# Performance work log

Measured on AMD Instinct MI355X. Metric: run time of the kernel, lower is better.

Reference implementation:

```python
import jax, jax.numpy as jnp
import numpy as np
from itertools import combinations

ADD = 3  # matches init_kwargs

def setup_inputs() -> dict:
    key = jax.random.key(0)
    x = jax.random.uniform(key, (131072, 16), dtype=jnp.float32)
    return {"x": x}

def reference(x) -> jnp.ndarray:
    n = x.shape[1]
    parts = [x]
    for i in range(2, ADD + 1):
        # static index table of all size-i column subsets: [C(n,i), i]
        idx = jnp.asarray(np.array(list(combinations(range(n), i)), dtype=np.int32))
        # gather + reduce: x[:, idx] -> [N, C, i]; Lukasiewicz t-norm = max(sum - (i-1), 0)
        s = jnp.sum(x[:, idx], axis=2)  # [N, C]
        parts.append(jnp.maximum(s - jnp.float32(i - 1), jnp.float32(0)))
    return jnp.concatenate(parts, axis=1)
```

## Files before the change

### kernel.cpp

```cpp
#include <hip/hip_runtime.h>


#define NCOLS 696
#define NC4   174
#define RPT   16
#define QPT   (RPT * NC4)

typedef float v4f __attribute__((ext_vector_type(4)));

struct ColTab { unsigned int v[NCOLS]; };

constexpr ColTab make_tab() {
    ColTab t{};
    int k = 0;
    for (int a = 0; a < 16; ++a)
        t.v[k++] = (unsigned)a | (16u << 5) | (16u << 10);
    for (int a = 0; a < 16; ++a)
        for (int b = a + 1; b < 16; ++b)
            t.v[k++] = (unsigned)a | ((unsigned)b << 5) | (16u << 10) | (1u << 15);
    for (int a = 0; a < 16; ++a)
        for (int b = a + 1; b < 16; ++b)
            for (int c = b + 1; c < 16; ++c)
                t.v[k++] = (unsigned)a | ((unsigned)b << 5) | ((unsigned)c << 10) | (2u << 15);
    return t;
}

__constant__ ColTab g_tab = make_tab();

__device__ __forceinline__ float tnorm(const float* __restrict__ xr, unsigned v) {
    return fmaxf(xr[v & 31u] + xr[(v >> 5) & 31u] + xr[(v >> 10) & 31u]
                 - (float)((v >> 15) & 3u), 0.0f);
}

__global__ __launch_bounds__(256) void luk_kernel(const float* __restrict__ x,
                                                  float* __restrict__ out,
                                                  int nrows, int ntiles) {
    __shared__ float xl[RPT * 17];
    const int t = threadIdx.x;
    const uint4* __restrict__ tab4 = reinterpret_cast<const uint4*>(g_tab.v);
    v4f* __restrict__ out4 = reinterpret_cast<v4f*>(out);

    for (int tile = blockIdx.x; tile < ntiles; tile += gridDim.x) {
        const int row0 = tile * RPT;
        const int rlim = min(RPT, nrows - row0);

        {
            const int r = t >> 4, a = t & 15;
            float v = 0.0f;
            if (r < rlim) v = x[(size_t)row0 * 16 + t];
            xl[r * 17 + a] = v;
            if (t < RPT) xl[t * 17 + 16] = 0.0f;
        }
        __syncthreads();

        const int nq = rlim * NC4;
        const size_t qbase = (size_t)row0 * NC4;
        for (int i = t; i < nq; i += 256) {
            const int r  = (unsigned)i / (unsigned)NC4;
            const int c4 = i - r * NC4;
            const uint4 tv = tab4[c4];
            const float* __restrict__ xr = &xl[r * 17];
            v4f o;
            o.x = tnorm(xr, tv.x);
            o.y = tnorm(xr, tv.y);
            o.z = tnorm(xr, tv.z);
            o.w = tnorm(xr, tv.w);
            out4[qbase + i] = o;
        }
        __syncthreads();
    }
}

extern "C" void kernel_launch(void* const* d_in, const int* in_sizes, int n_in,
                              void* d_out, int out_size, void* d_ws, size_t ws_size,
                              hipStream_t stream) {
    const float* x = (const float*)d_in[0];
    float* out = (float*)d_out;
    const int nrows  = in_sizes[0] / 16;
    const int ntiles = (nrows + RPT - 1) / RPT;
    const int blocks = ntiles < 2048 ? ntiles : 2048;
    luk_kernel<<<blocks, 256, 0, stream>>>(x, out, nrows, ntiles);
}
```

Measured before the change: 372.9 us.

## Compute one row per thread in registers with compile-time column table and LDS transpose

Each thread now loads its whole 16-float row into registers. All 696 outputs are generated through template-unrolled compile-time index tables, which removes the per-element table lookups, indirect LDS reads and integer division. Results are staged per wave in LDS in groups of 32 columns and transposed, so stores go out as contiguous 128-byte segments. The grid is now one thread per row, with no bounds check, so it assumes the row count is a multiple of 256. Code size and register use rise.

New measurement: 447.9 us. 20.1% more time.

```diff
diff --git a/kernel.cpp b/kernel.cpp
--- a/kernel.cpp
+++ b/kernel.cpp
@@ -3,72 +3,88 @@
 
 #define NCOLS 696
 #define NC4   174
-#define RPT   16
-#define QPT   (RPT * NC4)
+#define NG    22
 
 typedef float v4f __attribute__((ext_vector_type(4)));
 
-struct ColTab { unsigned int v[NCOLS]; };
-
-constexpr ColTab make_tab() {
-    ColTab t{};
+struct Tabs { signed char a[NCOLS], b[NCOLS], c[NCOLS], t[NCOLS]; };
+constexpr Tabs make_tabs() {
+    Tabs T{};
     int k = 0;
+    for (int a = 0; a < 16; ++a) {
+        T.a[k] = (signed char)a; T.b[k] = 0; T.c[k] = 0; T.t[k] = 0; ++k;
+    }
     for (int a = 0; a < 16; ++a)
-        t.v[k++] = (unsigned)a | (16u << 5) | (16u << 10);
+        for (int b = a + 1; b < 16; ++b) {
+            T.a[k] = (signed char)a; T.b[k] = (signed char)b; T.c[k] = 0; T.t[k] = 1; ++k;
+        }
     for (int a = 0; a < 16; ++a)
         for (int b = a + 1; b < 16; ++b)
-            t.v[k++] = (unsigned)a | ((unsigned)b << 5) | (16u << 10) | (1u << 15);
-    for (int a = 0; a < 16; ++a)
-        for (int b = a + 1; b < 16; ++b)
-            for (int c = b + 1; c < 16; ++c)
-                t.v[k++] = (unsigned)a | ((unsigned)b << 5) | ((unsigned)c << 10) | (2u << 15);
-    return t;
+            for (int c = b + 1; c < 16; ++c) {
+                T.a[k] = (signed char)a; T.b[k] = (signed char)b;
+                T.c[k] = (signed char)c; T.t[k] = 2; ++k;
+            }
+    return T;
+}
+constexpr Tabs TT = make_tabs();
+
+template<int COL>
+__device__ __forceinline__ float elem(const float* __restrict__ xr) {
+    constexpr int A = TT.a[COL], B = TT.b[COL], C = TT.c[COL], TY = TT.t[COL];
+    if constexpr (TY == 0)      return xr[A];
+    else if constexpr (TY == 1) return fmaxf(xr[A] + xr[B] - 1.0f, 0.0f);
+    else                        return fmaxf((xr[A] + xr[B]) + xr[C] - 2.0f, 0.0f);
 }
 
-__constant__ ColTab g_tab = make_tab();
+template<int G, int J, int NQ>
+__device__ __forceinline__ void compute_quads(const float* __restrict__ xr,
+                                              v4f* __restrict__ slab, int lane) {
+    if constexpr (J < NQ) {
+        constexpr int col0 = 32 * G + 4 * J;
+        v4f o;
+        o.x = elem<col0 + 0>(xr);
+        o.y = elem<col0 + 1>(xr);
+        o.z = elem<col0 + 2>(xr);
+        o.w = elem<col0 + 3>(xr);
+        slab[J * 64 + lane] = o;
+        compute_quads<G, J + 1, NQ>(xr, slab, lane);
+    }
+}
 
-__device__ __forceinline__ float tnorm(const float* __restrict__ xr, unsigned v) {
-    return fmaxf(xr[v & 31u] + xr[(v >> 5) & 31u] + xr[(v >> 10) & 31u]
-                 - (float)((v >> 15) & 3u), 0.0f);
+template<int G>
+__device__ __forceinline__ void do_group(const float* __restrict__ xr,
+                                         v4f* __restrict__ slab, int lane,
+                                         v4f* __restrict__ blk4, int voffq) {
+    constexpr int NQ = (G < 21) ? 8 : 6;
+    compute_quads<G, 0, NQ>(xr, slab, lane);
+    #pragma unroll
+    for (int m = 0; m < 8; ++m) {
+        const v4f o = slab[(lane & 7) * 64 + m * 8 + (lane >> 3)];
+        if (NQ == 8 || (lane & 7) < NQ)
+            blk4[voffq + m * (8 * NC4) + G * 8] = o;
+    }
+    if constexpr (G + 1 < NG) do_group<G + 1>(xr, slab, lane, blk4, voffq);
 }
 
 __global__ __launch_bounds__(256) void luk_kernel(const float* __restrict__ x,
                                                   float* __restrict__ out,
-                                                  int nrows, int ntiles) {
-    __shared__ float xl[RPT * 17];
+                                                  int nrows) {
+    __shared__ v4f slab[4][8 * 64];
     const int t = threadIdx.x;
-    const uint4* __restrict__ tab4 = reinterpret_cast<const uint4*>(g_tab.v);
-    v4f* __restrict__ out4 = reinterpret_cast<v4f*>(out);
+    const int w = t >> 6, lane = t & 63;
+    const int row0 = blockIdx.x * 256 + w * 64;
+    const int row  = row0 + lane;
 
-    for (int tile = blockIdx.x; tile < ntiles; tile += gridDim.x) {
-        const int row0 = tile * RPT;
-        const int rlim = min(RPT, nrows - row0);
+    float xr[16];
+    const v4f* __restrict__ xv = reinterpret_cast<const v4f*>(x) + (size_t)row * 4;
+    *reinterpret_cast<v4f*>(&xr[0])  = xv[0];
+    *reinterpret_cast<v4f*>(&xr[4])  = xv[1];
+    *reinterpret_cast<v4f*>(&xr[8])  = xv[2];
+    *reinterpret_cast<v4f*>(&xr[12]) = xv[3];
 
-        {
-            const int r = t >> 4, a = t & 15;
-            float v = 0.0f;
-            if (r < rlim) v = x[(size_t)row0 * 16 + t];
-            xl[r * 17 + a] = v;
-            if (t < RPT) xl[t * 17 + 16] = 0.0f;
-        }
-        __syncthreads();
-
-        const int nq = rlim * NC4;
-        const size_t qbase = (size_t)row0 * NC4;
-        for (int i = t; i < nq; i += 256) {
-            const int r  = (unsigned)i / (unsigned)NC4;
-            const int c4 = i - r * NC4;
-            const uint4 tv = tab4[c4];
-            const float* __restrict__ xr = &xl[r * 17];
-            v4f o;
-            o.x = tnorm(xr, tv.x);
-            o.y = tnorm(xr, tv.y);
-            o.z = tnorm(xr, tv.z);
-            o.w = tnorm(xr, tv.w);
-            out4[qbase + i] = o;
-        }
-        __syncthreads();
-    }
+    v4f* __restrict__ blk4 = reinterpret_cast<v4f*>(out) + (size_t)row0 * NC4;
+    const int voffq = (lane >> 3) * NC4 + (lane & 7);
+    do_group<0>(xr, slab[w], lane, blk4, voffq);
 }
 
 extern "C" void kernel_launch(void* const* d_in, const int* in_sizes, int n_in,
@@ -77,7 +93,6 @@
     const float* x = (const float*)d_in[0];
     float* out = (float*)d_out;
     const int nrows  = in_sizes[0] / 16;
-    const int ntiles = (nrows + RPT - 1) / RPT;
-    const int blocks = ntiles < 2048 ? ntiles : 2048;
-    luk_kernel<<<blocks, 256, 0, stream>>>(x, out, nrows, ntiles);
+    const int blocks = nrows / 256;
+    luk_kernel<<<blocks, 256, 0, stream>>>(x, out, nrows);
 }
```

## Precompute pair sums in LDS and hoist per-thread column offsets into registers

Applied to the files above, without the earlier changes.

Each row's 120 pairwise sums are computed once into shared memory, and each triple is then evaluated as a pair sum plus a single column, so every output needs two LDS reads instead of three. Per-thread packed byte offsets and biases are computed once before the tile loop and held in registers, which removes the constant-table loads and the div/mod from the inner loop. The partial-tile handling is dropped, so correctness assumes the row count is a multiple of 16. This adds an extra barrier and phase per tile and raises register use.

New measurement: 368.2 us. About the same (-1.3%).

```diff
diff --git a/kernel.cpp b/kernel.cpp
--- a/kernel.cpp
+++ b/kernel.cpp
@@ -4,68 +4,119 @@
 #define NCOLS 696
 #define NC4   174
 #define RPT   16
-#define QPT   (RPT * NC4)
+#define RSTR  260
+#define ZOFF  256
+#define NQ    (RPT * NC4)
+#define KITER 11
 
 typedef float v4f __attribute__((ext_vector_type(4)));
 
-struct ColTab { unsigned int v[NCOLS]; };
-
-constexpr ColTab make_tab() {
-    ColTab t{};
+struct DTab { unsigned int v[NCOLS]; };
+constexpr DTab make_dtab() {
+    DTab d{};
+    int pidx[16][16] = {};
+    int pi = 0;
+    for (int a = 0; a < 16; ++a)
+        for (int b = a + 1; b < 16; ++b) pidx[a][b] = pi++;
     int k = 0;
     for (int a = 0; a < 16; ++a)
-        t.v[k++] = (unsigned)a | (16u << 5) | (16u << 10);
+        d.v[k++] = (unsigned)(a * 4) | ((unsigned)(ZOFF * 4) << 16);
     for (int a = 0; a < 16; ++a)
         for (int b = a + 1; b < 16; ++b)
-            t.v[k++] = (unsigned)a | ((unsigned)b << 5) | (16u << 10) | (1u << 15);
+            d.v[k++] = (unsigned)((136 + pidx[a][b]) * 4) | ((unsigned)(ZOFF * 4) << 16);
     for (int a = 0; a < 16; ++a)
         for (int b = a + 1; b < 16; ++b)
             for (int c = b + 1; c < 16; ++c)
-                t.v[k++] = (unsigned)a | ((unsigned)b << 5) | ((unsigned)c << 10) | (2u << 15);
-    return t;
+                d.v[k++] = (unsigned)((16 + pidx[a][b]) * 4) | ((unsigned)(c * 4) << 16);
+    return d;
 }
+__constant__ DTab g_dtab = make_dtab();
 
-__constant__ ColTab g_tab = make_tab();
+struct PTab { unsigned short v[120]; };
+constexpr PTab make_ptab() {
+    PTab p{};
+    int k = 0;
+    for (int a = 0; a < 16; ++a)
+        for (int b = a + 1; b < 16; ++b)
+            p.v[k++] = (unsigned short)((a * 4) | ((b * 4) << 8));
+    return p;
+}
+__constant__ PTab g_ptab = make_ptab();
 
-__device__ __forceinline__ float tnorm(const float* __restrict__ xr, unsigned v) {
-    return fmaxf(xr[v & 31u] + xr[(v >> 5) & 31u] + xr[(v >> 10) & 31u]
-                 - (float)((v >> 15) & 3u), 0.0f);
+__device__ __forceinline__ float ldsf(const char* Lb, unsigned off) {
+    return *reinterpret_cast<const float*>(Lb + off);
 }
 
 __global__ __launch_bounds__(256) void luk_kernel(const float* __restrict__ x,
                                                   float* __restrict__ out,
-                                                  int nrows, int ntiles) {
-    __shared__ float xl[RPT * 17];
+                                                  int ntiles) {
+    __shared__ float L[RPT * RSTR];
     const int t = threadIdx.x;
-    const uint4* __restrict__ tab4 = reinterpret_cast<const uint4*>(g_tab.v);
-    v4f* __restrict__ out4 = reinterpret_cast<v4f*>(out);
+
+    unsigned pk[KITER][4];
+    float    nb[KITER];
+    #pragma unroll
+    for (int k = 0; k < KITER; ++k) {
+        const int i = t + 256 * k;
+        if (i < NQ) {
+            const unsigned r  = (unsigned)i / (unsigned)NC4;
+            const int      c4 = i - (int)r * NC4;
+            const unsigned radd = (r * (unsigned)(RSTR * 4)) * 0x10001u;
+            const uint4 dv = reinterpret_cast<const uint4*>(g_dtab.v)[c4];
+            pk[k][0] = dv.x + radd;
+            pk[k][1] = dv.y + radd;
+            pk[k][2] = dv.z + radd;
+            pk[k][3] = dv.w + radd;
+            nb[k] = (c4 < 34) ? 0.0f : -2.0f;
+        } else {
+            pk[k][0] = pk[k][1] = pk[k][2] = pk[k][3] = 0;
+            nb[k] = 0.0f;
+        }
+    }
+
+    const char* __restrict__ Lb = reinterpret_cast<const char*>(L);
 
     for (int tile = blockIdx.x; tile < ntiles; tile += gridDim.x) {
         const int row0 = tile * RPT;
-        const int rlim = min(RPT, nrows - row0);
 
         {
             const int r = t >> 4, a = t & 15;
-            float v = 0.0f;
-            if (r < rlim) v = x[(size_t)row0 * 16 + t];
-            xl[r * 17 + a] = v;
-            if (t < RPT) xl[t * 17 + 16] = 0.0f;
+            L[r * RSTR + a] = x[(size_t)row0 * 16 + t];
+            if (t < RPT) L[t * RSTR + ZOFF] = 0.0f;
         }
         __syncthreads();
 
-        const int nq = rlim * NC4;
-        const size_t qbase = (size_t)row0 * NC4;
-        for (int i = t; i < nq; i += 256) {
-            const int r  = (unsigned)i / (unsigned)NC4;
-            const int c4 = i - r * NC4;
-            const uint4 tv = tab4[c4];
-            const float* __restrict__ xr = &xl[r * 17];
-            v4f o;
-            o.x = tnorm(xr, tv.x);
-            o.y = tnorm(xr, tv.y);
-            o.z = tnorm(xr, tv.z);
-            o.w = tnorm(xr, tv.w);
-            out4[qbase + i] = o;
+        #pragma unroll
+        for (int m = 0; m < 8; ++m) {
+            const int j = t + 256 * m;
+            if (m < 7 || j < RPT * 120) {
+                const unsigned r = (unsigned)j / 120u;
+                const int      p = j - (int)r * 120;
+                const unsigned pv = g_ptab.v[p];
+                const char* xr = reinterpret_cast<const char*>(&L[r * RSTR]);
+                const float ps = ldsf(xr, pv & 255u) + ldsf(xr, pv >> 8);
+                L[r * RSTR + 16 + p]  = ps;
+                L[r * RSTR + 136 + p] = ps - 1.0f;
+            }
+        }
+        __syncthreads();
+
+        v4f* __restrict__ o4 = reinterpret_cast<v4f*>(out + (size_t)row0 * NCOLS);
+        #pragma unroll
+        for (int k = 0; k < KITER; ++k) {
+            if (k < KITER - 1 || t < NQ - 256 * (KITER - 1)) {
+                const float nbk = nb[k];
+                v4f o;
+                { const unsigned p0 = pk[k][0];
+                  o.x = fmaxf((ldsf(Lb, p0 & 0xffffu) + ldsf(Lb, p0 >> 16)) + nbk, 0.0f); }
+                { const unsigned p1 = pk[k][1];
+                  o.y = fmaxf((ldsf(Lb, p1 & 0xffffu) + ldsf(Lb, p1 >> 16)) + nbk, 0.0f); }
+                { const unsigned p2 = pk[k][2];
+                  o.z = fmaxf((ldsf(Lb, p2 & 0xffffu) + ldsf(Lb, p2 >> 16)) + nbk, 0.0f); }
+                { const unsigned p3 = pk[k][3];
+                  o.w = fmaxf((ldsf(Lb, p3 & 0xffffu) + ldsf(Lb, p3 >> 16)) + nbk, 0.0f); }
+                o4[t + 256 * k] = o;
+            }
         }
         __syncthreads();
     }
@@ -77,7 +128,7 @@
     const float* x = (const float*)d_in[0];
     float* out = (float*)d_out;
     const int nrows  = in_sizes[0] / 16;
-    const int ntiles = (nrows + RPT - 1) / RPT;
+    const int ntiles = nrows / RPT;
     const int blocks = ntiles < 2048 ? ntiles : 2048;
-    luk_kernel<<<blocks, 256, 0, stream>>>(x, out, nrows, ntiles);
+    luk_kernel<<<blocks, 256, 0, stream>>>(x, out, ntiles);
 }
```

## Assign one 16-row tile per wavefront and drop block-level barriers

Applied to the files above, without the earlier changes.

Each 64-lane wavefront now owns its own 16-row tile with a private shared-memory slab, so the two __syncthreads per tile are gone. The persistent grid-stride loop is replaced by one tile per wave, launching ntiles/4 blocks. Input loads become 16-byte vector loads into a row stride of 20. In exchange each wave writes a contiguous 44 KB output chunk with less parallelism per tile, and the grid is much larger.

After: 365.1 us (median of 2 runs). 1.02x faster.

```diff
diff --git a/kernel.cpp b/kernel.cpp
--- a/kernel.cpp
+++ b/kernel.cpp
@@ -4,7 +4,7 @@
 #define NCOLS 696
 #define NC4   174
 #define RPT   16
-#define QPT   (RPT * NC4)
+#define RSTR  20
 
 typedef float v4f __attribute__((ext_vector_type(4)));
 
@@ -35,39 +35,45 @@
 __global__ __launch_bounds__(256) void luk_kernel(const float* __restrict__ x,
                                                   float* __restrict__ out,
                                                   int nrows, int ntiles) {
-    __shared__ float xl[RPT * 17];
+    __shared__ float slabs[4][RPT * RSTR];
     const int t = threadIdx.x;
+    const int w = t >> 6, lane = t & 63;
+    const int tile = blockIdx.x * 4 + w;
+    if (tile >= ntiles) return;
+
+    float* __restrict__ slab = slabs[w];
+    const int row0 = tile * RPT;
+    const int rlim = min(RPT, nrows - row0);
+
+    {
+        const int r  = lane >> 2;
+        const int c0 = (lane & 3) * 4;
+        v4f v = {0.0f, 0.0f, 0.0f, 0.0f};
+        if (r < rlim)
+            v = *reinterpret_cast<const v4f*>(x + (size_t)(row0 + r) * 16 + c0);
+        *reinterpret_cast<v4f*>(&slab[r * RSTR + c0]) = v;
+        if (lane < RPT) slab[lane * RSTR + 16] = 0.0f;
+    }
+
     const uint4* __restrict__ tab4 = reinterpret_cast<const uint4*>(g_tab.v);
-    v4f* __restrict__ out4 = reinterpret_cast<v4f*>(out);
+    v4f* __restrict__ o4 = reinterpret_cast<v4f*>(out) + (size_t)tile * (RPT * NC4);
+    const int nq = rlim * NC4;
 
-    for (int tile = blockIdx.x; tile < ntiles; tile += gridDim.x) {
-        const int row0 = tile * RPT;
-        const int rlim = min(RPT, nrows - row0);
-
-        {
-            const int r = t >> 4, a = t & 15;
-            float v = 0.0f;
-            if (r < rlim) v = x[(size_t)row0 * 16 + t];
-            xl[r * 17 + a] = v;
-            if (t < RPT) xl[t * 17 + 16] = 0.0f;
-        }
-        __syncthreads();
-
-        const int nq = rlim * NC4;
-        const size_t qbase = (size_t)row0 * NC4;
-        for (int i = t; i < nq; i += 256) {
-            const int r  = (unsigned)i / (unsigned)NC4;
-            const int c4 = i - r * NC4;
+    #pragma unroll 4
+    for (int j = 0; j < (RPT * NC4 + 63) / 64; ++j) {
+        const int q = j * 64 + lane;
+        if (q < nq) {
+            const unsigned r  = (unsigned)q / (unsigned)NC4;
+            const int      c4 = q - (int)r * NC4;
             const uint4 tv = tab4[c4];
-            const float* __restrict__ xr = &xl[r * 17];
+            const float* __restrict__ xr = &slab[r * RSTR];
             v4f o;
             o.x = tnorm(xr, tv.x);
             o.y = tnorm(xr, tv.y);
             o.z = tnorm(xr, tv.z);
             o.w = tnorm(xr, tv.w);
-            out4[qbase + i] = o;
+            o4[q] = o;
         }
-        __syncthreads();
     }
 }
 
@@ -78,6 +84,6 @@
     float* out = (float*)d_out;
     const int nrows  = in_sizes[0] / 16;
     const int ntiles = (nrows + RPT - 1) / RPT;
-    const int blocks = ntiles < 2048 ? ntiles : 2048;
+    const int blocks = (ntiles + 3) / 4;
     luk_kernel<<<blocks, 256, 0, stream>>>(x, out, nrows, ntiles);
 }
```
